# Kernel tuning notes

Hardware: AMD Instinct MI355X
Metric: run time of the kernel (lower is better)

## Reference

```python
import jax, jax.numpy as jnp
import numpy as np

NUM_EMBEDDINGS = 16384
EMBEDDING_DIM = 512
COMMITMENT_COST = 0.25  # legacy: vq_loss = commit + beta * codebook
NORM_EPS = 1e-12  # F.normalize default eps


def setup_inputs() -> dict:
    key = jax.random.key(0)
    k_z, k_emb, k_w, k_b = jax.random.split(key, 4)
    z = jax.random.normal(k_z, (8, 1024, EMBEDDING_DIM), dtype=jnp.float32)
    # frozen codebook, init normal with std = D^{-0.5}
    embedding_weight = jax.random.normal(k_emb, (NUM_EMBEDDINGS, EMBEDDING_DIM), dtype=jnp.float32) * (EMBEDDING_DIM ** -0.5)
    # learnable projection (torch Linear: y = x @ W.T + b, W is [out, in])
    bound = 1.0 / np.sqrt(EMBEDDING_DIM)
    proj_w = jax.random.uniform(k_w, (EMBEDDING_DIM, EMBEDDING_DIM), dtype=jnp.float32, minval=-bound, maxval=bound)
    proj_b = jax.random.uniform(k_b, (EMBEDDING_DIM,), dtype=jnp.float32, minval=-bound, maxval=bound)
    scale = jnp.asarray(10.0, dtype=jnp.float32)
    return {"z": z, "embedding_weight": embedding_weight, "proj_w": proj_w, "proj_b": proj_b, "scale": scale}


def _l2_normalize(x):
    n = jnp.linalg.norm(x, axis=-1, keepdims=True)
    return x / jnp.maximum(n, NORM_EPS)


def reference(z, embedding_weight, proj_w, proj_b, scale):
    B, N, D = z.shape
    z_flat = z.reshape(-1, D)                                   # [M, D]
    quant_codebook = embedding_weight @ proj_w.T + proj_b       # [K, D]
    z_n = _l2_normalize(z_flat)
    c_n = _l2_normalize(quant_codebook)
    distances = -(z_n @ c_n.T) * scale                          # [M, K]
    encoding_indices = jnp.argmin(distances, axis=1)            # [M]
    quantized = quant_codebook[encoding_indices].reshape(z.shape)
    commitment_loss = jnp.mean((jax.lax.stop_gradient(quantized) - z) ** 2)
    codebook_loss = jnp.mean((quantized - jax.lax.stop_gradient(z)) ** 2)
    vq_loss = commitment_loss + COMMITMENT_COST * codebook_loss  # legacy=True
    quantized = z + jax.lax.stop_gradient(quantized - z)         # straight-through
    encoding_indices = encoding_indices.reshape(B, N)
    return quantized, vq_loss, encoding_indices
```

## Files before the change

### kernel.cpp

```cpp
#include <hip/hip_runtime.h>
#include <math.h>


typedef _Float16 f16;
typedef _Float16 f16x8 __attribute__((ext_vector_type(8)));
typedef _Float16 f16x4 __attribute__((ext_vector_type(4)));
typedef short s16x8 __attribute__((ext_vector_type(8)));
typedef float f32x4 __attribute__((ext_vector_type(4)));
typedef unsigned int u32;
typedef unsigned long long u64;
typedef unsigned short ushort_t;

#define INV2048 (1.0f/2048.0f)
#define MARGIN  0.010f

#define OFF_Q    0u
#define OFF_EHI  33554432u
#define OFF_ELO  50331648u
#define OFF_WHI  67108864u
#define OFF_WLO  67633152u
#define OFF_CB   68157440u
#define OFF_ZB   84934656u
#define OFF_RL   93323264u
#define OFF_PK   OFF_EHI

__device__ __forceinline__ void gload_lds16(const void* g, void* l) {
  __builtin_amdgcn_global_load_lds(
      (const __attribute__((address_space(1))) u32*)g,
      (__attribute__((address_space(3))) u32*)l, 16, 0, 0);
}

__device__ __forceinline__ u64 make_key(float v, int idx) {
  u32 b = __float_as_uint(v);
  u32 m = (u32)((int)b >> 31) | 0x80000000u;
  return ((u64)(b ^ m) << 32) | (u32)(0x7FFFFFFF - idx);
}
__device__ __forceinline__ float key_val(u64 k) {
  u32 o = (u32)(k >> 32);
  u32 m = (o & 0x80000000u) ? 0x80000000u : 0xFFFFFFFFu;
  return __uint_as_float(o ^ m);
}
__device__ __forceinline__ int key_idx(u64 k) {
  return 0x7FFFFFFF - (int)(u32)(k & 0xFFFFFFFFu);
}
__device__ __forceinline__ u64 umax64(u64 a, u64 b) { return a > b ? a : b; }

#define LDS_AHI 0
#define LDS_ALO 16384
#define LDS_BHI 32768
#define LDS_BLO 49152

__device__ __forceinline__ void stage_tile(const void* __restrict__ src, int row0,
                                           int kt, char* lds, int tid) {
#pragma unroll
  for (int i = 0; i < 4; ++i) {
    int lin = i * 256 + tid;
    int row = lin >> 3;
    int slot = lin & 7;
    int k8 = slot ^ (row & 7);
    const char* g = (const char*)src + (((size_t)(row0 + row)) << 10)
                    + (size_t)(kt * 128 + k8 * 16);
    gload_lds16(g, lds + lin * 16);
  }
}

__global__ __launch_bounds__(256, 2) void k_gemm_codebook(
    const f16* __restrict__ Ahi, const f16* __restrict__ Alo,
    const f16* __restrict__ Bhi, const f16* __restrict__ Blo,
    const float* __restrict__ bias, float* __restrict__ Q) {
  __shared__ __align__(16) char lds[65536];
  f32x4 hh[4][4], xx[4][4];
  const int tid = threadIdx.x;
  const int m0 = blockIdx.y * 128;
  const int n0 = blockIdx.x * 128;
  const int l = tid & 63;
  const int wid = tid >> 6;
  const int wr = (wid >> 1) * 64;
  const int wc = (wid & 1) * 64;
  const int r7 = (l & 15) & 7;

#pragma unroll
  for (int a = 0; a < 4; ++a)
#pragma unroll
    for (int b = 0; b < 4; ++b) {
      hh[a][b] = (f32x4){0.f, 0.f, 0.f, 0.f};
      xx[a][b] = (f32x4){0.f, 0.f, 0.f, 0.f};
    }

  for (int kt = 0; kt < 8; ++kt) {
    stage_tile(Ahi, m0, kt, lds + LDS_AHI, tid);
    stage_tile(Alo, m0, kt, lds + LDS_ALO, tid);
    stage_tile(Bhi, n0, kt, lds + LDS_BHI, tid);
    stage_tile(Blo, n0, kt, lds + LDS_BLO, tid);
    __syncthreads();
#pragma unroll
    for (int ks = 0; ks < 2; ++ks) {
      const int kg = ks * 4 + (l >> 4);
      const int s = (kg ^ r7) * 16;
      const char* pa = lds + (wr + (l & 15)) * 128 + s;
      const char* pb = lds + (wc + (l & 15)) * 128 + s;
      f16x8 ahi[4], alo[4];
#pragma unroll
      for (int mf = 0; mf < 4; ++mf) {
        ahi[mf] = *(const f16x8*)(pa + LDS_AHI + mf * 2048);
        alo[mf] = *(const f16x8*)(pa + LDS_ALO + mf * 2048);
      }
#pragma unroll
      for (int nf = 0; nf < 4; ++nf) {
        f16x8 bhi = *(const f16x8*)(pb + LDS_BHI + nf * 2048);
        f16x8 blo = *(const f16x8*)(pb + LDS_BLO + nf * 2048);
#pragma unroll
        for (int mf = 0; mf < 4; ++mf) {
          hh[mf][nf] = __builtin_amdgcn_mfma_f32_16x16x32_f16(ahi[mf], bhi, hh[mf][nf], 0, 0, 0);
          xx[mf][nf] = __builtin_amdgcn_mfma_f32_16x16x32_f16(ahi[mf], blo, xx[mf][nf], 0, 0, 0);
          xx[mf][nf] = __builtin_amdgcn_mfma_f32_16x16x32_f16(alo[mf], bhi, xx[mf][nf], 0, 0, 0);
        }
      }
    }
    __syncthreads();
  }

#pragma unroll
  for (int mf = 0; mf < 4; ++mf)
#pragma unroll
    for (int nf = 0; nf < 4; ++nf)
#pragma unroll
      for (int j = 0; j < 4; ++j) {
        int row = m0 + wr + mf * 16 + (l >> 4) * 4 + j;
        int col = n0 + wc + nf * 16 + (l & 15);
        Q[(size_t)row * 512 + col] = hh[mf][nf][j] + xx[mf][nf][j] * INV2048 + bias[col];
      }
}

#define PHASE(CUR, KS, MFH, PF, STISA, STKS, WN)                               \
  {                                                                            \
    const char* base_ = lds + (CUR) * 65536 + (KS) * 16384;                    \
    if ((MFH) == 0) {                                                          \
      bfr[0] = *(const s16x8*)(base_ + boff + 0);                              \
      bfr[1] = *(const s16x8*)(base_ + boff + 256);                            \
      bfr[2] = *(const s16x8*)(base_ + boff + 512);                            \
      bfr[3] = *(const s16x8*)(base_ + boff + 768);                            \
    }                                                                          \
    s16x8 af0 = *(const s16x8*)(base_ + aoff + (MFH) * 1024 + 0);              \
    s16x8 af1 = *(const s16x8*)(base_ + aoff + (MFH) * 1024 + 256);            \
    s16x8 af2 = *(const s16x8*)(base_ + aoff + (MFH) * 1024 + 512);            \
    s16x8 af3 = *(const s16x8*)(base_ + aoff + (MFH) * 1024 + 768);            \
    if (PF) {                                                                  \
      char* d_ = lds + ((t & 1) ^ 1) * 65536 + ((STISA) ? 0 : 32768)           \
                 + (STKS) * 16384 + tid * 16;                                  \
      const char* g_ = ((STISA) ? srcA : srcB) + (t + 1) * 128 + (STKS) * 64;  \
      gload_lds16(g_, d_);                                                     \
      gload_lds16(g_ + 32, d_ + 8192);                                         \
    }                                                                          \
    __builtin_amdgcn_s_setprio(1);                                             \
    _Pragma("unroll") for (int nf = 0; nf < 4; ++nf) {                         \
      acc[(MFH)*4+0][nf] = __builtin_amdgcn_mfma_f32_16x16x32_bf16(af0, bfr[nf], acc[(MFH)*4+0][nf], 0, 0, 0); \
      acc[(MFH)*4+1][nf] = __builtin_amdgcn_mfma_f32_16x16x32_bf16(af1, bfr[nf], acc[(MFH)*4+1][nf], 0, 0, 0); \
      acc[(MFH)*4+2][nf] = __builtin_amdgcn_mfma_f32_16x16x32_bf16(af2, bfr[nf], acc[(MFH)*4+2][nf], 0, 0, 0); \
      acc[(MFH)*4+3][nf] = __builtin_amdgcn_mfma_f32_16x16x32_bf16(af3, bfr[nf], acc[(MFH)*4+3][nf], 0, 0, 0); \
    }                                                                          \
    __builtin_amdgcn_s_setprio(0);                                             \
    asm volatile("s_waitcnt vmcnt(" #WN ")\n\ts_barrier" ::: "memory");        \
  }

__global__ __launch_bounds__(512, 2) void k_gemm_coarse8(
    const ushort_t* __restrict__ CB, const ushort_t* __restrict__ ZB,
    u64* __restrict__ pk) {
  __shared__ __align__(16) char lds[131072];
  const int tid = threadIdx.x;
  const int l = tid & 63;
  const int wid = tid >> 6;
  const int wr = wid >> 2;
  const int wc = wid & 3;
  const int cb0 = blockIdx.x * 256;
  const int zb0 = blockIdx.y * 256;

  const int srow = tid & 255, skg = tid >> 8;
  const char* srcA = (const char*)CB + (((size_t)(cb0 + srow)) << 10) + skg * 16;
  const char* srcB = (const char*)ZB + (((size_t)(zb0 + srow)) << 10) + skg * 16;

  const int lane_off = (l >> 4) * 4096 + (l & 15) * 16;
  const int aoff = wr * 2048 + lane_off;
  const int boff = 32768 + wc * 1024 + lane_off;

  f32x4 acc[8][4];
#pragma unroll
  for (int a = 0; a < 8; ++a)
#pragma unroll
    for (int b = 0; b < 4; ++b) acc[a][b] = (f32x4){0.f, 0.f, 0.f, 0.f};

  {
    char* d;
    const char* g;
    d = lds + 0 + tid * 16;        g = srcA + 0;         gload_lds16(g, d); gload_lds16(g + 32, d + 8192);
    d = lds + 32768 + tid * 16;    g = srcB + 0;         gload_lds16(g, d); gload_lds16(g + 32, d + 8192);
    d = lds + 16384 + tid * 16;    g = srcA + 64;        gload_lds16(g, d); gload_lds16(g + 32, d + 8192);
    d = lds + 49152 + tid * 16;    g = srcB + 64;        gload_lds16(g, d); gload_lds16(g + 32, d + 8192);
    asm volatile("s_waitcnt vmcnt(4)\n\ts_barrier" ::: "memory");
  }

  s16x8 bfr[4];
  for (int t = 0; t < 7; ++t) {
    const int cur = t & 1;
    PHASE(cur, 0, 0, true, 1, 0, 4)
    PHASE(cur, 0, 1, true, 0, 0, 4)
    PHASE(cur, 1, 0, true, 1, 1, 4)
    PHASE(cur, 1, 1, true, 0, 1, 4)
  }
  {
    const int t = 7;
    (void)t;
    PHASE(1, 0, 0, false, 1, 0, 2)
    PHASE(1, 0, 1, false, 0, 0, 0)
    PHASE(1, 1, 0, false, 1, 1, 0)
    PHASE(1, 1, 1, false, 0, 1, 0)
  }

  float* cmax = (float*)lds;
  u32* cnt = (u32*)(lds + 2048);
  u64* slots = (u64*)(lds + 4096);

  float cm[4];
#pragma unroll
  for (int nf = 0; nf < 4; ++nf) {
    float m = acc[0][nf][0];
#pragma unroll
    for (int mfa = 0; mfa < 8; ++mfa)
#pragma unroll
      for (int j = 0; j < 4; ++j) m = fmaxf(m, acc[mfa][nf][j]);
    m = fmaxf(m, __shfl_xor(m, 16, 64));
    m = fmaxf(m, __shfl_xor(m, 32, 64));
    cm[nf] = m;
  }
  if (tid < 256) cnt[tid] = 0;
  slots[tid] = 0;
  slots[tid + 512] = 0;
  if ((l >> 4) == 0) {
#pragma unroll
    for (int nf = 0; nf < 4; ++nf)
      cmax[(wc * 64 + nf * 16 + l) * 2 + wr] = cm[nf];
  }
  __syncthreads();

#pragma unroll
  for (int nf = 0; nf < 4; ++nf) {
    int col = wc * 64 + nf * 16 + (l & 15);
    float thresh = fmaxf(cmax[col * 2], cmax[col * 2 + 1]) - MARGIN;
#pragma unroll
    for (int mfa = 0; mfa < 8; ++mfa)
#pragma unroll
      for (int j = 0; j < 4; ++j) {
        float v = acc[mfa][nf][j];
        if (v >= thresh) {
          int code = cb0 + wr * 128 + mfa * 16 + ((l >> 4) << 2) + j;
          u32 p = atomicAdd(&cnt[col], 1u);
          if (p < 4) slots[col * 4 + p] = make_key(v, code);
        }
      }
  }
  __syncthreads();

  if (tid < 256) {
    size_t base = (((size_t)(zb0 + tid)) * 64 + blockIdx.x) * 4;
#pragma unroll
    for (int s = 0; s < 4; ++s) pk[base + s] = slots[tid * 4 + s];
  }
}

__global__ __launch_bounds__(256) void k_split(const float* __restrict__ src,
                                               f16* __restrict__ hi,
                                               f16* __restrict__ lo, int n4) {
  int i = blockIdx.x * 256 + threadIdx.x;
  if (i >= n4) return;
  const float4 v = ((const float4*)src)[i];
  f16 h0 = (f16)v.x, h1 = (f16)v.y, h2 = (f16)v.z, h3 = (f16)v.w;
  ((f16x4*)hi)[i] = (f16x4){h0, h1, h2, h3};
  ((f16x4*)lo)[i] = (f16x4){(f16)((v.x - (float)h0) * 2048.0f),
                            (f16)((v.y - (float)h1) * 2048.0f),
                            (f16)((v.z - (float)h2) * 2048.0f),
                            (f16)((v.w - (float)h3) * 2048.0f)};
}

__device__ __forceinline__ ushort_t f2bf_rne(float f) {
  u32 b = __float_as_uint(f);
  b += 0x7FFFu + ((b >> 16) & 1u);
  return (ushort_t)(b >> 16);
}

__global__ __launch_bounds__(256) void k_norm_bf16(const float* __restrict__ src,
                                                   ushort_t* __restrict__ dst) {
  __shared__ float red[256];
  const int row = blockIdx.x, t = threadIdx.x;
  float q0 = src[(size_t)row * 512 + t];
  float q1 = src[(size_t)row * 512 + t + 256];
  red[t] = q0 * q0 + q1 * q1;
  __syncthreads();
  for (int s = 128; s > 0; s >>= 1) {
    if (t < s) red[t] += red[t + s];
    __syncthreads();
  }
  float inv = 1.0f / fmaxf(sqrtf(red[0]), 1e-12f);
  dst[(size_t)row * 512 + t] = f2bf_rne(q0 * inv);
  dst[(size_t)row * 512 + t + 256] = f2bf_rne(q1 * inv);
}

__global__ __launch_bounds__(256) void k_rescore_gather(
    const u64* __restrict__ pk, const float* __restrict__ Q,
    const float* __restrict__ z, float* __restrict__ outq,
    float* __restrict__ outidx, float* __restrict__ rloss) {
  __shared__ float sz[512];
  __shared__ double redd[8];
  __shared__ u64 redk[4];
  __shared__ int cand[64];
  __shared__ int ccount;
  const int row = blockIdx.x, t = threadIdx.x;

  sz[t] = z[(size_t)row * 512 + t];
  sz[t + 256] = z[(size_t)row * 512 + t + 256];
  if (t == 0) ccount = 0;

  u64 k1 = pk[(size_t)row * 256 + t];
  u64 km = k1;
  for (int m = 1; m < 64; m <<= 1)
    km = umax64(km, (u64)__shfl_xor((long long)km, m));
  if ((t & 63) == 0) redk[t >> 6] = km;
  __syncthreads();
  u64 gk = umax64(umax64(redk[0], redk[1]), umax64(redk[2], redk[3]));
  float thresh = key_val(gk) - MARGIN;

  if (key_val(k1) >= thresh) { int p = atomicAdd(&ccount, 1); if (p < 64) cand[p] = key_idx(k1); }
  __syncthreads();
  int nc = ccount < 64 ? ccount : 64;

  double bs = -1e300;
  int bi = 0x7FFFFFFF;
  for (int c = 0; c < nc; ++c) {
    int code = cand[c];
    const float* Qr = Q + (size_t)code * 512;
    double dotp = 0.0, qq = 0.0;
#pragma unroll
    for (int h = 0; h < 2; ++h) {
      int d = t + h * 256;
      double qv = (double)Qr[d];
      dotp += (double)sz[d] * qv;
      qq += qv * qv;
    }
    for (int m = 1; m < 64; m <<= 1) {
      dotp += __shfl_xor(dotp, m);
      qq += __shfl_xor(qq, m);
    }
    if ((t & 63) == 0) { redd[t >> 6] = dotp; redd[4 + (t >> 6)] = qq; }
    __syncthreads();
    double dsum = redd[0] + redd[1] + redd[2] + redd[3];
    double qsum = redd[4] + redd[5] + redd[6] + redd[7];
    double s = dsum / fmax(sqrt(qsum), 1e-12);
    if (s > bs || (s == bs && code < bi)) { bs = s; bi = code; }
    __syncthreads();
  }

  const float* Qb = Q + (size_t)bi * 512;
  double lsum = 0.0;
#pragma unroll
  for (int h = 0; h < 2; ++h) {
    int d = t + h * 256;
    float qv = Qb[d], zv = sz[d];
    outq[(size_t)row * 512 + d] = zv + (qv - zv);
    float df = qv - zv;
    lsum += (double)df * (double)df;
  }
  for (int m = 1; m < 64; m <<= 1) lsum += __shfl_xor(lsum, m);
  if ((t & 63) == 0) redd[t >> 6] = lsum;
  __syncthreads();
  if (t == 0) {
    rloss[row] = (float)(redd[0] + redd[1] + redd[2] + redd[3]);
    outidx[row] = (float)bi;
  }
}

__global__ __launch_bounds__(256) void k_loss_final(const float* __restrict__ rloss,
                                                    float* __restrict__ out_loss) {
  __shared__ float sl[256];
  int t = threadIdx.x;
  float s = 0.f;
#pragma unroll
  for (int i = 0; i < 32; ++i) s += rloss[t + i * 256];
  sl[t] = s;
  __syncthreads();
  for (int k = 128; k > 0; k >>= 1) {
    if (t < k) sl[t] += sl[t + k];
    __syncthreads();
  }
  if (t == 0) out_loss[0] = 1.25f * sl[0] / 4194304.0f;
}

extern "C" void kernel_launch(void* const* d_in, const int* in_sizes, int n_in,
                              void* d_out, int out_size, void* d_ws, size_t ws_size,
                              hipStream_t stream) {
  const float* z = (const float*)d_in[0];
  const float* emb = (const float*)d_in[1];
  const float* pw = (const float*)d_in[2];
  const float* pb = (const float*)d_in[3];

  char* ws = (char*)d_ws;
  float* Q = (float*)(ws + OFF_Q);
  f16* ehi = (f16*)(ws + OFF_EHI);
  f16* elo = (f16*)(ws + OFF_ELO);
  f16* whi = (f16*)(ws + OFF_WHI);
  f16* wlo = (f16*)(ws + OFF_WLO);
  ushort_t* cb = (ushort_t*)(ws + OFF_CB);
  ushort_t* zb = (ushort_t*)(ws + OFF_ZB);
  u64* pk = (u64*)(ws + OFF_PK);
  float* rloss = (float*)(ws + OFF_RL);

  float* outq = (float*)d_out;
  float* outloss = outq + 4194304;
  float* outidx = outq + 4194305;

  k_split<<<8192, 256, 0, stream>>>(emb, ehi, elo, 2097152);
  k_split<<<256, 256, 0, stream>>>(pw, whi, wlo, 65536);
  k_norm_bf16<<<8192, 256, 0, stream>>>(z, zb);
  k_gemm_codebook<<<dim3(4, 128), 256, 0, stream>>>(ehi, elo, whi, wlo, pb, Q);
  k_norm_bf16<<<16384, 256, 0, stream>>>(Q, cb);
  k_gemm_coarse8<<<dim3(64, 32), 512, 0, stream>>>(cb, zb, pk);
  k_rescore_gather<<<8192, 256, 0, stream>>>(pk, Q, z, outq, outidx, rloss);
  k_loss_final<<<1, 256, 0, stream>>>(rloss, outloss);
}
```

Measured before the change: 352.8 us.

## Use XOR-swizzled row-major LDS layout and batch prefetch in the coarse GEMM

Changes how codebook and z tiles are staged in LDS. Each row now occupies 128 contiguous bytes, with the 16-byte chunk index XOR-swizzled by the row, and fragment reads use matching swizzled offsets. This is meant to cut LDS bank conflicts and make the global loads more contiguous. All eight async global-to-LDS loads for the next K-tile are now issued in the first phase, with vmcnt waits moved to the last two phases, and the main loop is fully unrolled with a predicated prefetch. The trade-off is a different overlap pattern and possibly higher register or instruction pressure.

```diff
diff --git a/kernel.cpp b/kernel.cpp
--- a/kernel.cpp
+++ b/kernel.cpp
@@ -132,25 +132,36 @@
       }
 }
 
-#define PHASE(CUR, KS, MFH, PF, STISA, STKS, WN)                               \
+#define BAR() __builtin_amdgcn_s_barrier()
+
+#define PHASE(CUR, KS, MFH, PF, SYNC)                                          \
   {                                                                            \
-    const char* base_ = lds + (CUR) * 65536 + (KS) * 16384;                    \
+    const char* abase_ = lds + (CUR) * 65536;                                  \
     if ((MFH) == 0) {                                                          \
-      bfr[0] = *(const s16x8*)(base_ + boff + 0);                              \
-      bfr[1] = *(const s16x8*)(base_ + boff + 256);                            \
-      bfr[2] = *(const s16x8*)(base_ + boff + 512);                            \
-      bfr[3] = *(const s16x8*)(base_ + boff + 768);                            \
+      const char* pb_ = abase_ + 32768 + boff + ((KS) ? s1 : s0);              \
+      bfr[0] = *(const s16x8*)(pb_ + 0);                                       \
+      bfr[1] = *(const s16x8*)(pb_ + 2048);                                    \
+      bfr[2] = *(const s16x8*)(pb_ + 4096);                                    \
+      bfr[3] = *(const s16x8*)(pb_ + 6144);                                    \
     }                                                                          \
-    s16x8 af0 = *(const s16x8*)(base_ + aoff + (MFH) * 1024 + 0);              \
-    s16x8 af1 = *(const s16x8*)(base_ + aoff + (MFH) * 1024 + 256);            \
-    s16x8 af2 = *(const s16x8*)(base_ + aoff + (MFH) * 1024 + 512);            \
-    s16x8 af3 = *(const s16x8*)(base_ + aoff + (MFH) * 1024 + 768);            \
-    if (PF) {                                                                  \
-      char* d_ = lds + ((t & 1) ^ 1) * 65536 + ((STISA) ? 0 : 32768)           \
-                 + (STKS) * 16384 + tid * 16;                                  \
-      const char* g_ = ((STISA) ? srcA : srcB) + (t + 1) * 128 + (STKS) * 64;  \
-      gload_lds16(g_, d_);                                                     \
-      gload_lds16(g_ + 32, d_ + 8192);                                         \
+    const char* pa_ = abase_ + aoff + (MFH) * 8192 + ((KS) ? s1 : s0);         \
+    s16x8 af0 = *(const s16x8*)(pa_ + 0);                                      \
+    s16x8 af1 = *(const s16x8*)(pa_ + 2048);                                   \
+    s16x8 af2 = *(const s16x8*)(pa_ + 4096);                                   \
+    s16x8 af3 = *(const s16x8*)(pa_ + 6144);                                   \
+    if (PF) {         \
+      char* dA_ = lds + ((CUR) ^ 1) * 65536 + tid * 16;                        \
+      const char* gA_ = srcA + (t + 1) * 128;                                  \
+      gload_lds16(gA_, dA_);                                                   \
+      gload_lds16(gA_ + 65536, dA_ + 8192);                                    \
+      gload_lds16(gA_ + 131072, dA_ + 16384);                                  \
+      gload_lds16(gA_ + 196608, dA_ + 24576);                                  \
+      char* dB_ = dA_ + 32768;                                                 \
+      const char* gB_ = srcB + (t + 1) * 128;                                  \
+      gload_lds16(gB_, dB_);                                                   \
+      gload_lds16(gB_ + 65536, dB_ + 8192);                                    \
+      gload_lds16(gB_ + 131072, dB_ + 16384);                                  \
+      gload_lds16(gB_ + 196608, dB_ + 24576);                                  \
     }                                                                          \
     __builtin_amdgcn_s_setprio(1);                                             \
     _Pragma("unroll") for (int nf = 0; nf < 4; ++nf) {                         \
@@ -160,7 +171,7 @@
       acc[(MFH)*4+3][nf] = __builtin_amdgcn_mfma_f32_16x16x32_bf16(af3, bfr[nf], acc[(MFH)*4+3][nf], 0, 0, 0); \
     }                                                                          \
     __builtin_amdgcn_s_setprio(0);                                             \
-    asm volatile("s_waitcnt vmcnt(" #WN ")\n\ts_barrier" ::: "memory");        \
+    SYNC;                                                                      \
   }
 
 __global__ __launch_bounds__(512, 2) void k_gemm_coarse8(
@@ -175,13 +186,15 @@
   const int cb0 = blockIdx.x * 256;
   const int zb0 = blockIdx.y * 256;
 
-  const int srow = tid & 255, skg = tid >> 8;
-  const char* srcA = (const char*)CB + (((size_t)(cb0 + srow)) << 10) + skg * 16;
-  const char* srcB = (const char*)ZB + (((size_t)(zb0 + srow)) << 10) + skg * 16;
-
-  const int lane_off = (l >> 4) * 4096 + (l & 15) * 16;
-  const int aoff = wr * 2048 + lane_off;
-  const int boff = 32768 + wc * 1024 + lane_off;
+  const int k8 = (tid & 7) ^ ((tid >> 3) & 7);
+  const char* srcA = (const char*)CB + (((size_t)(cb0 + (tid >> 3))) << 10) + k8 * 16;
+  const char* srcB = (const char*)ZB + (((size_t)(zb0 + (tid >> 3))) << 10) + k8 * 16;
+
+  const int r7 = (l & 15) & 7;
+  const int s0 = (((l >> 4)) ^ r7) * 16;
+  const int s1 = (((l >> 4) | 4) ^ r7) * 16;
+  const int aoff = wr * 16384 + (l & 15) * 128;
+  const int boff = wc * 8192 + (l & 15) * 128;
 
   f32x4 acc[8][4];
 #pragma unroll
@@ -190,30 +203,29 @@
     for (int b = 0; b < 4; ++b) acc[a][b] = (f32x4){0.f, 0.f, 0.f, 0.f};
 
   {
-    char* d;
-    const char* g;
-    d = lds + 0 + tid * 16;        g = srcA + 0;         gload_lds16(g, d); gload_lds16(g + 32, d + 8192);
-    d = lds + 32768 + tid * 16;    g = srcB + 0;         gload_lds16(g, d); gload_lds16(g + 32, d + 8192);
-    d = lds + 16384 + tid * 16;    g = srcA + 64;        gload_lds16(g, d); gload_lds16(g + 32, d + 8192);
-    d = lds + 49152 + tid * 16;    g = srcB + 64;        gload_lds16(g, d); gload_lds16(g + 32, d + 8192);
-    asm volatile("s_waitcnt vmcnt(4)\n\ts_barrier" ::: "memory");
+    char* dA_ = lds + tid * 16;
+    gload_lds16(srcA, dA_);
+    gload_lds16(srcA + 65536, dA_ + 8192);
+    gload_lds16(srcA + 131072, dA_ + 16384);
+    gload_lds16(srcA + 196608, dA_ + 24576);
+    char* dB_ = dA_ + 32768;
+    gload_lds16(srcB, dB_);
+    gload_lds16(srcB + 65536, dB_ + 8192);
+    gload_lds16(srcB + 131072, dB_ + 16384);
+    gload_lds16(srcB + 196608, dB_ + 24576);
+    asm volatile("s_waitcnt vmcnt(0)" ::: "memory");
+    BAR();
   }
 
   s16x8 bfr[4];
-  for (int t = 0; t < 7; ++t) {
+#pragma unroll
+  for (int t = 0; t < 8; ++t) {
     const int cur = t & 1;
-    PHASE(cur, 0, 0, true, 1, 0, 4)
-    PHASE(cur, 0, 1, true, 0, 0, 4)
-    PHASE(cur, 1, 0, true, 1, 1, 4)
-    PHASE(cur, 1, 1, true, 0, 1, 4)
-  }
-  {
-    const int t = 7;
-    (void)t;
-    PHASE(1, 0, 0, false, 1, 0, 2)
-    PHASE(1, 0, 1, false, 0, 0, 0)
-    PHASE(1, 1, 0, false, 1, 1, 0)
-    PHASE(1, 1, 1, false, 0, 1, 0)
+    const bool pf = (t < 7);
+    PHASE(cur, 0, 0, pf, BAR())
+    PHASE(cur, 0, 1, false, BAR())
+    PHASE(cur, 1, 0, false, { asm volatile("s_waitcnt vmcnt(4)" ::: "memory"); BAR(); })
+    PHASE(cur, 1, 1, false, { asm volatile("s_waitcnt vmcnt(0)" ::: "memory"); BAR(); })
   }
 
   float* cmax = (float*)lds;
```

After: 300.6 us. 1.17x faster.
